# Kernel tuning notes

Measured on AMD Instinct MI355X. Metric: run time of the kernel, lower is better.

## Reference

```python
import jax, jax.numpy as jnp
import numpy as np

N_TOK = 16384   # total tokens (batch*seq)
H = 2048        # hidden_size
I = 768         # moe_intermediate_size (per-expert MLP width)
TOPK = 8        # num_experts_per_tok


def setup_inputs() -> dict:
    key = jax.random.key(0)
    ks = jax.random.split(key, 7)
    hidden_states = jax.random.normal(ks[0], (N_TOK, H), dtype=jnp.float32)
    # expert_mask[j, k] != 0 means token k selected this expert at top-k slot j
    expert_mask = jax.random.randint(ks[1], (TOPK, N_TOK), 0, 2, dtype=jnp.int32)
    routing_weights = jax.random.uniform(ks[2], (N_TOK, TOPK), dtype=jnp.float32)
    final_hidden_states = jax.random.normal(ks[3], (N_TOK, H), dtype=jnp.float32)
    gate_w = jax.random.normal(ks[4], (I, H), dtype=jnp.float32) * 0.02
    up_w = jax.random.normal(ks[5], (I, H), dtype=jnp.float32) * 0.02
    down_w = jax.random.normal(ks[6], (H, I), dtype=jnp.float32) * 0.02
    return {
        "hidden_states": hidden_states,
        "expert_mask": expert_mask,
        "routing_weights": routing_weights,
        "final_hidden_states": final_hidden_states,
        "gate_w": gate_w,
        "up_w": up_w,
        "down_w": down_w,
    }


def reference(hidden_states, expert_mask, routing_weights, final_hidden_states,
              gate_w, up_w, down_w):
    # forward_expert: gather selected tokens, SwiGLU MLP, scale by routing weight,
    # scatter-add into final_hidden_states. Equivalent jit-friendly form: the
    # combined routing weight per token is w[k] = sum_j mask[j,k]*routing_weights[k,j]
    # (tokens selected multiple times are summed, matching index_add_ semantics),
    # and unselected tokens get w[k]=0 so they contribute nothing.
    g = hidden_states @ gate_w.T                       # [N, I]
    u = hidden_states @ up_w.T                         # [N, I]
    y = (jax.nn.silu(g) * u) @ down_w.T                # [N, H]
    w = jnp.einsum('jk,kj->k', expert_mask.astype(y.dtype), routing_weights)  # [N]
    return final_hidden_states + y * w[:, None]
```

## Files before the change

### kernel.cpp

```cpp
#include <hip/hip_runtime.h>
#include <stdint.h>

#define NTOK 16384
#define HD   2048
#define ID   768
#define TOPK 8

typedef __bf16 bf16x8 __attribute__((ext_vector_type(8)));
typedef float  floatx4 __attribute__((ext_vector_type(4)));
typedef unsigned short ushort8 __attribute__((ext_vector_type(8)));

__device__ __forceinline__ unsigned short f32_to_bf16_rne(float f) {
    union { float f; uint32_t u; } v; v.f = f;
    uint32_t u = v.u;
    u += 0x7FFFu + ((u >> 16) & 1u);
    return (unsigned short)(u >> 16);
}
__device__ __forceinline__ float bf16_to_f32(unsigned short h) {
    union { uint32_t u; float f; } v; v.u = ((uint32_t)h) << 16;
    return v.f;
}

#define GLD_LDS(gsrc, ldst)                                                              \
    __builtin_amdgcn_global_load_lds(                                                    \
        (const __attribute__((address_space(1))) uint32_t*)(const void*)(gsrc),          \
        (__attribute__((address_space(3))) uint32_t*)(void*)(ldst), 16, 0, 0)

template<int VM> __device__ __forceinline__ void wait_vm() {
    if constexpr (VM == 4)      asm volatile("s_waitcnt vmcnt(4)" ::: "memory");
    else if constexpr (VM == 3) asm volatile("s_waitcnt vmcnt(3)" ::: "memory");
    else                        asm volatile("s_waitcnt vmcnt(0)" ::: "memory");
}
#define BARRIER() do { asm volatile("" ::: "memory");              \
                       __builtin_amdgcn_s_barrier();               \
                       asm volatile("" ::: "memory"); } while (0)

__global__ __launch_bounds__(256) void compute_w_kernel(const int* __restrict__ mask,
                                                        const float* __restrict__ rw,
                                                        float* __restrict__ w) {
    int k = blockIdx.x * 256 + threadIdx.x;
    if (k >= NTOK) return;
    float acc = 0.f;
#pragma unroll
    for (int j = 0; j < TOPK; ++j)
        acc += (float)mask[j * NTOK + k] * rw[k * TOPK + j];
    w[k] = acc;
}

__global__ __launch_bounds__(256) void convert_hs_kernel(const float* __restrict__ src,
                                                         unsigned short* __restrict__ dst) {
    size_t i = (size_t)blockIdx.x * 256 + threadIdx.x;
    const float4* s = (const float4*)src;
    float4 a = s[2 * i], b = s[2 * i + 1];
    ushort8 o;
    o[0] = f32_to_bf16_rne(a.x); o[1] = f32_to_bf16_rne(a.y);
    o[2] = f32_to_bf16_rne(a.z); o[3] = f32_to_bf16_rne(a.w);
    o[4] = f32_to_bf16_rne(b.x); o[5] = f32_to_bf16_rne(b.y);
    o[6] = f32_to_bf16_rne(b.z); o[7] = f32_to_bf16_rne(b.w);
    *(ushort8*)(dst + 8 * i) = o;
}

__global__ __launch_bounds__(256) void convert_w3_kernel(const float* __restrict__ g,
                                                         const float* __restrict__ u,
                                                         const float* __restrict__ d,
                                                         unsigned short* __restrict__ dst) {
    const int per = ID * HD / 8;
    int i = blockIdx.x * 256 + threadIdx.x;
    int which = i / per;
    int off = i - which * per;
    const float* src = (which == 0) ? g : ((which == 1) ? u : d);
    const float4* s = (const float4*)src;
    float4 a = s[2 * (size_t)off], b = s[2 * (size_t)off + 1];
    ushort8 o;
    o[0] = f32_to_bf16_rne(a.x); o[1] = f32_to_bf16_rne(a.y);
    o[2] = f32_to_bf16_rne(a.z); o[3] = f32_to_bf16_rne(a.w);
    o[4] = f32_to_bf16_rne(b.x); o[5] = f32_to_bf16_rne(b.y);
    o[6] = f32_to_bf16_rne(b.z); o[7] = f32_to_bf16_rne(b.w);
    *(ushort8*)(dst + 8 * (size_t)i) = o;
}

__global__ __launch_bounds__(256) void swiglu_kernel(const unsigned short* __restrict__ gu,
                                                     unsigned short* __restrict__ act) {
    int i = blockIdx.x * 256 + threadIdx.x;
    int t = i / (ID / 8);
    int c8 = i - t * (ID / 8);
    ushort8 g = *(const ushort8*)&gu[(size_t)t * (2 * ID) + c8 * 8];
    ushort8 u = *(const ushort8*)&gu[(size_t)t * (2 * ID) + ID + c8 * 8];
    ushort8 o;
#pragma unroll
    for (int j = 0; j < 8; ++j) {
        float gf = bf16_to_f32(g[j]);
        float uf = bf16_to_f32(u[j]);
        float s = gf / (1.f + __expf(-gf)) * uf;
        o[j] = f32_to_bf16_rne(s);
    }
    *(ushort8*)&act[(size_t)t * ID + c8 * 8] = o;
}

__global__ __launch_bounds__(512, 1) void gemm_gu_kernel(
    const unsigned short* __restrict__ A,
    const unsigned short* __restrict__ B,
    unsigned short* __restrict__ Cb) {
    constexpr int K = HD;
    constexpr int NT = K / 64;
    __shared__ __align__(16) unsigned char lds[2][57344];

    const int bid = blockIdx.x, nwg = gridDim.x;
    const int nb = (bid & 7) * (nwg >> 3) + (bid >> 3);
    const int bx = nb & 7, by = nb >> 3;
    const int row0 = by * 256, col0 = bx * 192;

    const int tid = threadIdx.x, wid = tid >> 6, lane = tid & 63;
    const int wr = wid >> 2, wc = wid & 3;
    const int lrow = lane & 15, q = lane >> 4;
    const int rsw = ((q ^ ((lrow >> 1) & 3)) << 4);

    const int kswz = (((lane & 3) ^ ((lane >> 3) & 3)) << 3);
    const unsigned short* sA[2];
#pragma unroll
    for (int h = 0; h < 2; ++h) {
        const int o = h * 8192 + wid * 1024 + lane * 16;
        sA[h] = A + (size_t)(row0 + (o >> 6)) * K + kswz;
    }
    const unsigned short* sB[3];
#pragma unroll
    for (int r = 0; r < 3; ++r) {
        const int o = r * 8192 + tid * 16;
        const int ks = (o >= 12288) ? 1 : 0;
        const int brow = (o - ks * 12288) >> 6;
        sB[r] = B + (size_t)(col0 + brow) * K + ks * 32 + kswz;
    }

#define STAGE_A(sb, ks, kt) do {                                                            \
        GLD_LDS(sA[0] + (kt) * 64 + (ks) * 32, lds[sb] + (ks) * 16384 + wid * 1024);        \
        GLD_LDS(sA[1] + (kt) * 64 + (ks) * 32, lds[sb] + (ks) * 16384 + 8192 + wid * 1024); \
    } while (0)
#define STAGE_B01(sb, kt) do {                                                              \
        GLD_LDS(sB[0] + (kt) * 64, lds[sb] + 32768 + wid * 1024);                           \
        GLD_LDS(sB[1] + (kt) * 64, lds[sb] + 32768 + 8192 + wid * 1024);                    \
    } while (0)
#define STAGE_B2(sb, kt)                                                                    \
        GLD_LDS(sB[2] + (kt) * 64, lds[sb] + 32768 + 16384 + wid * 1024)

#define READ_A(s, ks) do { const unsigned char* rgn = lds[s] + (ks) * 16384;                \
        _Pragma("unroll")                                                                   \
        for (int m = 0; m < 8; ++m)                                                         \
            af[m] = *(const bf16x8*)(rgn + (wr * 128 + m * 16 + lrow) * 64 + rsw);          \
    } while (0)
#define READ_B(s, ks) do { const unsigned char* rgn = lds[s] + 32768 + (ks) * 12288;        \
        _Pragma("unroll")                                                                   \
        for (int n = 0; n < 3; ++n)                                                         \
            bb[n] = *(const bf16x8*)(rgn + (wc * 48 + n * 16 + lrow) * 64 + rsw);           \
    } while (0)
#define MFMA_H(mh) do {                                                                     \
        __builtin_amdgcn_s_setprio(1);                                                      \
        _Pragma("unroll")                                                                   \
        for (int m = (mh) * 4; m < (mh) * 4 + 4; ++m)                                       \
            _Pragma("unroll")                                                               \
            for (int n = 0; n < 3; ++n)                                                     \
                acc[m][n] = __builtin_amdgcn_mfma_f32_16x16x32_bf16(af[m], bb[n], acc[m][n], 0, 0, 0); \
        __builtin_amdgcn_s_setprio(0);                                                      \
    } while (0)

    floatx4 acc[8][3];
#pragma unroll
    for (int m = 0; m < 8; ++m)
#pragma unroll
        for (int n = 0; n < 3; ++n) acc[m][n] = (floatx4){0.f, 0.f, 0.f, 0.f};
    bf16x8 af[8], bb[3];

    STAGE_A(0, 0, 0);
    STAGE_B01(0, 0);
    STAGE_A(0, 1, 0);
    STAGE_B2(0, 0);
    wait_vm<3>();
    BARRIER();

    for (int t = 0; t < NT - 1; ++t) {
        const int s = t & 1, sn = s ^ 1;
        READ_A(s, 0); READ_B(s, 0);
        STAGE_A(sn, 0, t + 1);
        MFMA_H(0);
        BARRIER();
        STAGE_B01(sn, t + 1);
        MFMA_H(1);
        wait_vm<4>();
        BARRIER();
        READ_A(s, 1); READ_B(s, 1);
        STAGE_A(sn, 1, t + 1);
        MFMA_H(0);
        BARRIER();
        STAGE_B2(sn, t + 1);
        MFMA_H(1);
        wait_vm<3>();
        BARRIER();
    }
    {
        const int s = (NT - 1) & 1;
        READ_A(s, 0); READ_B(s, 0);
        MFMA_H(0);
        BARRIER();
        MFMA_H(1);
        wait_vm<0>();
        BARRIER();
        READ_A(s, 1); READ_B(s, 1);
        MFMA_H(0);
        MFMA_H(1);
    }
#undef STAGE_A
#undef STAGE_B01
#undef STAGE_B2
#undef READ_A
#undef READ_B
#undef MFMA_H

#pragma unroll
    for (int m = 0; m < 8; ++m)
#pragma unroll
        for (int r = 0; r < 4; ++r) {
            const int row = row0 + wr * 128 + m * 16 + q * 4 + r;
#pragma unroll
            for (int n = 0; n < 3; ++n) {
                const int col = col0 + wc * 48 + n * 16 + lrow;
                Cb[(size_t)row * (2 * ID) + col] = f32_to_bf16_rne(acc[m][n][r]);
            }
        }
}

template<int K, int NC, bool FUSE_DOWN>
__global__ __launch_bounds__(512, 2) void gemm8p_kernel(
    const unsigned short* __restrict__ A,
    const unsigned short* __restrict__ B,
    unsigned short* __restrict__ Cb,
    const float* __restrict__ fin,
    const float* __restrict__ wtok,
    float* __restrict__ Cf) {
    constexpr int NT = K / 64;
    static_assert(NT >= 2, "");
    __shared__ __align__(16) unsigned short lds[2][4][8192];

    const int bid = blockIdx.x, nwg = gridDim.x;
    const int nb = (bid & 7) * (nwg >> 3) + (bid >> 3);
    const int bx = nb >> 6, by = nb & 63;
    const int row0 = by * 256, col0 = bx * 256;

    const int tid = threadIdx.x, wid = tid >> 6, lane = tid & 63;
    const int wr = wid >> 2, wc = wid & 3;
    const int lrow = lane & 15, q = lane >> 4;
    const int rsw = (((lrow >> 1) & 3) ^ q) << 4;

    const int srow = wid * 16 + (lane >> 2);
    const int kswz = (((lane & 3) ^ ((lane >> 3) & 3)) << 3);
    const unsigned short* sA0 = A + (size_t)(row0 + srow) * K + kswz;
    const unsigned short* sA1 = A + (size_t)(row0 + 128 + srow) * K + kswz;
    const unsigned short* sB0 = B + (size_t)(col0 + srow) * K + kswz;
    const unsigned short* sB1 = B + (size_t)(col0 + 128 + srow) * K + kswz;

#define STAGE(sb, reg, p0, p1, koff) do {                                   \
        GLD_LDS((p0) + (koff), &lds[sb][reg][wid * 512]);                   \
        GLD_LDS((p1) + (koff), &lds[sb][reg][4096 + wid * 512]);            \
    } while (0)

#define READ_A(ks) do { const unsigned short* rgn = &lds[s][(ks) * 2][0];   \
        _Pragma("unroll")                                                   \
        for (int m = 0; m < 8; ++m) {                                       \
            const int rl = wr * 128 + m * 16 + lrow;                        \
            af[m] = *(const bf16x8*)((const char*)rgn + rl * 64 + rsw);     \
        } } while (0)

#define READ_B(ks, nh) do { const unsigned short* rgn = &lds[s][(ks) * 2 + 1][0]; \
        _Pragma("unroll")                                                   \
        for (int n = 0; n < 2; ++n) {                                       \
            const int rl = wc * 64 + (nh) * 32 + n * 16 + lrow;             \
            bb[n] = *(const bf16x8*)((const char*)rgn + rl * 64 + rsw);     \
        } } while (0)

#define MFMA_Q(nh) do {                                                     \
        __builtin_amdgcn_s_setprio(1);                                      \
        _Pragma("unroll")                                                   \
        for (int m = 0; m < 8; ++m) {                                       \
            acc[m][(nh) * 2 + 0] = __builtin_amdgcn_mfma_f32_16x16x32_bf16(af[m], bb[0], acc[m][(nh) * 2 + 0], 0, 0, 0); \
            acc[m][(nh) * 2 + 1] = __builtin_amdgcn_mfma_f32_16x16x32_bf16(af[m], bb[1], acc[m][(nh) * 2 + 1], 0, 0, 0); \
        }                                                                   \
        __builtin_amdgcn_s_setprio(0);                                      \
    } while (0)

    floatx4 acc[8][4];
#pragma unroll
    for (int m = 0; m < 8; ++m)
#pragma unroll
        for (int n = 0; n < 4; ++n) acc[m][n] = (floatx4){0.f, 0.f, 0.f, 0.f};
    bf16x8 af[8], bb[2];

    STAGE(0, 0, sA0, sA1, 0);
    STAGE(0, 1, sB0, sB1, 0);
    STAGE(0, 2, sA0, sA1, 32);
    STAGE(0, 3, sB0, sB1, 32);
    wait_vm<4>();
    BARRIER();

    for (int t = 0; t < NT - 1; ++t) {
        const int s = t & 1, sn = s ^ 1;
        const int ko = (t + 1) * 64;
        READ_A(0); READ_B(0, 0);
        STAGE(sn, 0, sA0, sA1, ko);
        MFMA_Q(0);
        BARRIER();
        READ_B(0, 1);
        STAGE(sn, 1, sB0, sB1, ko);
        MFMA_Q(1);
        wait_vm<4>();
        BARRIER();
        READ_A(1); READ_B(1, 0);
        STAGE(sn, 2, sA0, sA1, ko + 32);
        MFMA_Q(0);
        BARRIER();
        READ_B(1, 1);
        STAGE(sn, 3, sB0, sB1, ko + 32);
        MFMA_Q(1);
        wait_vm<4>();
        BARRIER();
    }
    {
        const int s = (NT - 1) & 1;
        READ_A(0); READ_B(0, 0); MFMA_Q(0); BARRIER();
        READ_B(0, 1); MFMA_Q(1);
        wait_vm<0>();
        BARRIER();
        READ_A(1); READ_B(1, 0); MFMA_Q(0); BARRIER();
        READ_B(1, 1); MFMA_Q(1);
    }
#undef STAGE
#undef READ_A
#undef READ_B
#undef MFMA_Q

    if constexpr (!FUSE_DOWN) {
#pragma unroll
        for (int m = 0; m < 8; ++m)
#pragma unroll
            for (int r = 0; r < 4; ++r) {
                const int row = row0 + wr * 128 + m * 16 + q * 4 + r;
#pragma unroll
                for (int n = 0; n < 4; ++n) {
                    const int col = col0 + wc * 64 + n * 16 + lrow;
                    Cb[(size_t)row * NC + col] = f32_to_bf16_rne(acc[m][n][r]);
                }
            }
    } else {
#pragma unroll
        for (int m = 0; m < 8; ++m)
#pragma unroll
            for (int r = 0; r < 4; ++r) {
                const int row = row0 + wr * 128 + m * 16 + q * 4 + r;
                const float wv = wtok[row];
#pragma unroll
                for (int n = 0; n < 4; ++n) {
                    const int col = col0 + wc * 64 + n * 16 + lrow;
                    Cf[(size_t)row * NC + col] = fin[(size_t)row * NC + col] + wv * acc[m][n][r];
                }
            }
    }
}

extern "C" void kernel_launch(void* const* d_in, const int* in_sizes, int n_in,
                              void* d_out, int out_size, void* d_ws, size_t ws_size,
                              hipStream_t stream) {
    const float* hs   = (const float*)d_in[0];
    const int*   mask = (const int*)d_in[1];
    const float* rw   = (const float*)d_in[2];
    const float* fin  = (const float*)d_in[3];
    const float* gw   = (const float*)d_in[4];
    const float* uw   = (const float*)d_in[5];
    const float* dw   = (const float*)d_in[6];
    float* out = (float*)d_out;

    char* ws = (char*)d_ws;
    unsigned short* hs_b   = (unsigned short*)ws; ws += (size_t)NTOK * HD * 2;
    unsigned short* wcat_b = (unsigned short*)ws; ws += (size_t)3 * ID * HD * 2;
    unsigned short* gu_b   = (unsigned short*)ws; ws += (size_t)NTOK * 2 * ID * 2;
    float* wtok = (float*)ws;
    unsigned short* act_b = hs_b;
    unsigned short* down_b = wcat_b + (size_t)2 * ID * HD;

    compute_w_kernel<<<NTOK / 256, 256, 0, stream>>>(mask, rw, wtok);
    convert_hs_kernel<<<(NTOK * HD / 8) / 256, 256, 0, stream>>>(hs, hs_b);
    convert_w3_kernel<<<(3 * ID * HD / 8) / 256, 256, 0, stream>>>(gw, uw, dw, wcat_b);

    gemm_gu_kernel<<<512, 512, 0, stream>>>(hs_b, wcat_b, gu_b);

    swiglu_kernel<<<(NTOK * (ID / 8)) / 256, 256, 0, stream>>>(gu_b, act_b);

    gemm8p_kernel<ID, HD, true><<<(NTOK / 256) * (HD / 256), 512, 0, stream>>>(
        act_b, down_b, nullptr, fin, wtok, out);
}
```

Before: 243.2 us.

## Retile down GEMM to 128x128 blocks and split gate/up LDS reads

```diff
diff --git a/kernel.cpp b/kernel.cpp
--- a/kernel.cpp
+++ b/kernel.cpp
@@ -27,7 +27,8 @@
         (__attribute__((address_space(3))) uint32_t*)(void*)(ldst), 16, 0, 0)
 
 template<int VM> __device__ __forceinline__ void wait_vm() {
-    if constexpr (VM == 4)      asm volatile("s_waitcnt vmcnt(4)" ::: "memory");
+    if constexpr (VM == 8)      asm volatile("s_waitcnt vmcnt(8)" ::: "memory");
+    else if constexpr (VM == 7) asm volatile("s_waitcnt vmcnt(7)" ::: "memory");
     else if constexpr (VM == 3) asm volatile("s_waitcnt vmcnt(3)" ::: "memory");
     else                        asm volatile("s_waitcnt vmcnt(0)" ::: "memory");
 }
@@ -142,9 +143,14 @@
 #define STAGE_B2(sb, kt)                                                                    \
         GLD_LDS(sB[2] + (kt) * 64, lds[sb] + 32768 + 16384 + wid * 1024)
 
-#define READ_A(s, ks) do { const unsigned char* rgn = lds[s] + (ks) * 16384;                \
+#define READ_A03(s, ks) do { const unsigned char* rgn = lds[s] + (ks) * 16384;              \
         _Pragma("unroll")                                                                   \
-        for (int m = 0; m < 8; ++m)                                                         \
+        for (int m = 0; m < 4; ++m)                                                         \
+            af[m] = *(const bf16x8*)(rgn + (wr * 128 + m * 16 + lrow) * 64 + rsw);          \
+    } while (0)
+#define READ_A47(s, ks) do { const unsigned char* rgn = lds[s] + (ks) * 16384;              \
+        _Pragma("unroll")                                                                   \
+        for (int m = 4; m < 8; ++m)                                                         \
             af[m] = *(const bf16x8*)(rgn + (wr * 128 + m * 16 + lrow) * 64 + rsw);          \
     } while (0)
 #define READ_B(s, ks) do { const unsigned char* rgn = lds[s] + 32768 + (ks) * 12288;        \
@@ -178,39 +184,43 @@
 
     for (int t = 0; t < NT - 1; ++t) {
         const int s = t & 1, sn = s ^ 1;
-        READ_A(s, 0); READ_B(s, 0);
+        READ_B(s, 0); READ_A03(s, 0);
         STAGE_A(sn, 0, t + 1);
+        STAGE_B01(sn, t + 1);
         MFMA_H(0);
         BARRIER();
-        STAGE_B01(sn, t + 1);
-        MFMA_H(1);
-        wait_vm<4>();
-        BARRIER();
-        READ_A(s, 1); READ_B(s, 1);
+        READ_A47(s, 0);
         STAGE_A(sn, 1, t + 1);
-        MFMA_H(0);
-        BARRIER();
         STAGE_B2(sn, t + 1);
         MFMA_H(1);
+        wait_vm<7>();
+        BARRIER();
+        READ_B(s, 1); READ_A03(s, 1);
+        MFMA_H(0);
+        BARRIER();
+        READ_A47(s, 1);
+        MFMA_H(1);
         wait_vm<3>();
         BARRIER();
     }
     {
         const int s = (NT - 1) & 1;
-        READ_A(s, 0); READ_B(s, 0);
+        READ_B(s, 0); READ_A03(s, 0);
         MFMA_H(0);
-        BARRIER();
+        READ_A47(s, 0);
         MFMA_H(1);
         wait_vm<0>();
         BARRIER();
-        READ_A(s, 1); READ_B(s, 1);
+        READ_B(s, 1); READ_A03(s, 1);
         MFMA_H(0);
+        READ_A47(s, 1);
         MFMA_H(1);
     }
 #undef STAGE_A
 #undef STAGE_B01
 #undef STAGE_B2
-#undef READ_A
+#undef READ_A03
+#undef READ_A47
 #undef READ_B
 #undef MFMA_H
 
@@ -227,140 +237,98 @@
         }
 }
 
-template<int K, int NC, bool FUSE_DOWN>
-__global__ __launch_bounds__(512, 2) void gemm8p_kernel(
+__global__ __launch_bounds__(256, 2) void gemm_down_kernel(
     const unsigned short* __restrict__ A,
     const unsigned short* __restrict__ B,
-    unsigned short* __restrict__ Cb,
     const float* __restrict__ fin,
     const float* __restrict__ wtok,
-    float* __restrict__ Cf) {
+    float* __restrict__ out) {
+    constexpr int K = ID;
     constexpr int NT = K / 64;
-    static_assert(NT >= 2, "");
-    __shared__ __align__(16) unsigned short lds[2][4][8192];
+    __shared__ __align__(16) unsigned char lds[2][32768];
 
     const int bid = blockIdx.x, nwg = gridDim.x;
     const int nb = (bid & 7) * (nwg >> 3) + (bid >> 3);
-    const int bx = nb >> 6, by = nb & 63;
-    const int row0 = by * 256, col0 = bx * 256;
+    const int bx = nb & 15, by = nb >> 4;
+    const int row0 = by * 128, col0 = bx * 128;
 
     const int tid = threadIdx.x, wid = tid >> 6, lane = tid & 63;
-    const int wr = wid >> 2, wc = wid & 3;
+    const int wr = wid >> 1, wc = wid & 1;
     const int lrow = lane & 15, q = lane >> 4;
-    const int rsw = (((lrow >> 1) & 3) ^ q) << 4;
-
-    const int srow = wid * 16 + (lane >> 2);
-    const int kswz = (((lane & 3) ^ ((lane >> 3) & 3)) << 3);
-    const unsigned short* sA0 = A + (size_t)(row0 + srow) * K + kswz;
-    const unsigned short* sA1 = A + (size_t)(row0 + 128 + srow) * K + kswz;
-    const unsigned short* sB0 = B + (size_t)(col0 + srow) * K + kswz;
-    const unsigned short* sB1 = B + (size_t)(col0 + 128 + srow) * K + kswz;
-
-#define STAGE(sb, reg, p0, p1, koff) do {                                   \
-        GLD_LDS((p0) + (koff), &lds[sb][reg][wid * 512]);                   \
-        GLD_LDS((p1) + (koff), &lds[sb][reg][4096 + wid * 512]);            \
-    } while (0)
-
-#define READ_A(ks) do { const unsigned short* rgn = &lds[s][(ks) * 2][0];   \
-        _Pragma("unroll")                                                   \
-        for (int m = 0; m < 8; ++m) {                                       \
-            const int rl = wr * 128 + m * 16 + lrow;                        \
-            af[m] = *(const bf16x8*)((const char*)rgn + rl * 64 + rsw);     \
-        } } while (0)
-
-#define READ_B(ks, nh) do { const unsigned short* rgn = &lds[s][(ks) * 2 + 1][0]; \
-        _Pragma("unroll")                                                   \
-        for (int n = 0; n < 2; ++n) {                                       \
-            const int rl = wc * 64 + (nh) * 32 + n * 16 + lrow;             \
-            bb[n] = *(const bf16x8*)((const char*)rgn + rl * 64 + rsw);     \
-        } } while (0)
-
-#define MFMA_Q(nh) do {                                                     \
-        __builtin_amdgcn_s_setprio(1);                                      \
-        _Pragma("unroll")                                                   \
-        for (int m = 0; m < 8; ++m) {                                       \
-            acc[m][(nh) * 2 + 0] = __builtin_amdgcn_mfma_f32_16x16x32_bf16(af[m], bb[0], acc[m][(nh) * 2 + 0], 0, 0, 0); \
-            acc[m][(nh) * 2 + 1] = __builtin_amdgcn_mfma_f32_16x16x32_bf16(af[m], bb[1], acc[m][(nh) * 2 + 1], 0, 0, 0); \
-        }                                                                   \
-        __builtin_amdgcn_s_setprio(0);                                      \
-    } while (0)
-
-    floatx4 acc[8][4];
-#pragma unroll
-    for (int m = 0; m < 8; ++m)
+
+    const int srow = wid * 8 + (lane >> 3);
+    const int sk = (((lane & 7) ^ ((lane >> 3) & 7)) << 3);
+    const unsigned short* sA[4];
+    const unsigned short* sB[4];
+#pragma unroll
+    for (int r = 0; r < 4; ++r) {
+        sA[r] = A + (size_t)(row0 + r * 32 + srow) * K + sk;
+        sB[r] = B + (size_t)(col0 + r * 32 + srow) * K + sk;
+    }
+
+#define STAGE_T(sb, kt) do {                                                    \
+        _Pragma("unroll")                                                       \
+        for (int r = 0; r < 4; ++r)                                             \
+            GLD_LDS(sA[r] + (kt) * 64, lds[sb] + r * 4096 + wid * 1024);        \
+        _Pragma("unroll")                                                       \
+        for (int r = 0; r < 4; ++r)                                             \
+            GLD_LDS(sB[r] + (kt) * 64, lds[sb] + 16384 + r * 4096 + wid * 1024);\
+    } while (0)
+
+    floatx4 acc[4][4];
+#pragma unroll
+    for (int m = 0; m < 4; ++m)
 #pragma unroll
         for (int n = 0; n < 4; ++n) acc[m][n] = (floatx4){0.f, 0.f, 0.f, 0.f};
-    bf16x8 af[8], bb[2];
-
-    STAGE(0, 0, sA0, sA1, 0);
-    STAGE(0, 1, sB0, sB1, 0);
-    STAGE(0, 2, sA0, sA1, 32);
-    STAGE(0, 3, sB0, sB1, 32);
-    wait_vm<4>();
-    BARRIER();
-
-    for (int t = 0; t < NT - 1; ++t) {
-        const int s = t & 1, sn = s ^ 1;
-        const int ko = (t + 1) * 64;
-        READ_A(0); READ_B(0, 0);
-        STAGE(sn, 0, sA0, sA1, ko);
-        MFMA_Q(0);
-        BARRIER();
-        READ_B(0, 1);
-        STAGE(sn, 1, sB0, sB1, ko);
-        MFMA_Q(1);
-        wait_vm<4>();
-        BARRIER();
-        READ_A(1); READ_B(1, 0);
-        STAGE(sn, 2, sA0, sA1, ko + 32);
-        MFMA_Q(0);
-        BARRIER();
-        READ_B(1, 1);
-        STAGE(sn, 3, sB0, sB1, ko + 32);
-        MFMA_Q(1);
-        wait_vm<4>();
-        BARRIER();
-    }
-    {
-        const int s = (NT - 1) & 1;
-        READ_A(0); READ_B(0, 0); MFMA_Q(0); BARRIER();
-        READ_B(0, 1); MFMA_Q(1);
-        wait_vm<0>();
-        BARRIER();
-        READ_A(1); READ_B(1, 0); MFMA_Q(0); BARRIER();
-        READ_B(1, 1); MFMA_Q(1);
-    }
-#undef STAGE
-#undef READ_A
-#undef READ_B
-#undef MFMA_Q
-
-    if constexpr (!FUSE_DOWN) {
-#pragma unroll
-        for (int m = 0; m < 8; ++m)
-#pragma unroll
-            for (int r = 0; r < 4; ++r) {
-                const int row = row0 + wr * 128 + m * 16 + q * 4 + r;
-#pragma unroll
-                for (int n = 0; n < 4; ++n) {
-                    const int col = col0 + wc * 64 + n * 16 + lrow;
-                    Cb[(size_t)row * NC + col] = f32_to_bf16_rne(acc[m][n][r]);
-                }
+    bf16x8 af[4], bb[4];
+
+    STAGE_T(0, 0);
+
+    for (int t = 0; t < NT; ++t) {
+        const int s = t & 1;
+        if (t + 1 < NT) {
+            STAGE_T(s ^ 1, t + 1);
+            wait_vm<8>();
+        } else {
+            wait_vm<0>();
+        }
+        BARRIER();
+        const unsigned char* la = lds[s];
+        const unsigned char* lb = lds[s] + 16384;
+#pragma unroll
+        for (int ks = 0; ks < 2; ++ks) {
+#pragma unroll
+            for (int m = 0; m < 4; ++m)
+                af[m] = *(const bf16x8*)(la + (wr * 64 + m * 16 + lrow) * 128 +
+                                         (((ks * 4 + q) ^ (lrow & 7)) << 4));
+#pragma unroll
+            for (int n = 0; n < 4; ++n)
+                bb[n] = *(const bf16x8*)(lb + (wc * 64 + n * 16 + lrow) * 128 +
+                                         (((ks * 4 + q) ^ (lrow & 7)) << 4));
+            __builtin_amdgcn_s_setprio(1);
+#pragma unroll
+            for (int m = 0; m < 4; ++m)
+#pragma unroll
+                for (int n = 0; n < 4; ++n)
+                    acc[m][n] = __builtin_amdgcn_mfma_f32_16x16x32_bf16(af[m], bb[n], acc[m][n], 0, 0, 0);
+            __builtin_amdgcn_s_setprio(0);
+        }
+        BARRIER();
+    }
+#undef STAGE_T
+
+#pragma unroll
+    for (int m = 0; m < 4; ++m)
+#pragma unroll
+        for (int r = 0; r < 4; ++r) {
+            const int row = row0 + wr * 64 + m * 16 + q * 4 + r;
+            const float wv = wtok[row];
+#pragma unroll
+            for (int n = 0; n < 4; ++n) {
+                const int col = col0 + wc * 64 + n * 16 + lrow;
+                out[(size_t)row * HD + col] = fin[(size_t)row * HD + col] + wv * acc[m][n][r];
             }
-    } else {
-#pragma unroll
-        for (int m = 0; m < 8; ++m)
-#pragma unroll
-            for (int r = 0; r < 4; ++r) {
-                const int row = row0 + wr * 128 + m * 16 + q * 4 + r;
-                const float wv = wtok[row];
-#pragma unroll
-                for (int n = 0; n < 4; ++n) {
-                    const int col = col0 + wc * 64 + n * 16 + lrow;
-                    Cf[(size_t)row * NC + col] = fin[(size_t)row * NC + col] + wv * acc[m][n][r];
-                }
-            }
-    }
+        }
 }
 
 extern "C" void kernel_launch(void* const* d_in, const int* in_sizes, int n_in,
@@ -391,6 +359,5 @@
 
     swiglu_kernel<<<(NTOK * (ID / 8)) / 256, 256, 0, stream>>>(gu_b, act_b);
 
-    gemm8p_kernel<ID, HD, true><<<(NTOK / 256) * (HD / 256), 512, 0, stream>>>(
-        act_b, down_b, nullptr, fin, wtok, out);
-}
+    gemm_down_kernel<<<2048, 256, 0, stream>>>(act_b, down_b, fin, wtok, out);
+}
```

Measured after the change: 244.4 us. Within noise of the previous version (+0.5%).
